# Kernel tuning notes

Hardware: AMD Instinct MI355X
Metric: run time of the kernel (lower is better)

The kernel has to match this reference:

```python
import jax, jax.numpy as jnp
from jax import lax
import numpy as np

VOCAB, EMB, HID, NLAYERS, NCLS = 32000, 512, 1024, 2, 32000
B, T = 64, 256


def setup_inputs() -> dict:
    key = jax.random.key(0)
    ks = jax.random.split(key, 12)
    s_in = 1.0 / np.sqrt(HID)
    inp = {
        "tokens": jax.random.randint(ks[0], (B, T), 0, VOCAB),
        "emb": jax.random.normal(ks[1], (VOCAB, EMB), jnp.float32),
        "W_ih0": jax.random.uniform(ks[2], (4 * HID, EMB), jnp.float32, -s_in, s_in),
        "W_hh0": jax.random.uniform(ks[3], (4 * HID, HID), jnp.float32, -s_in, s_in),
        "b_ih0": jax.random.uniform(ks[4], (4 * HID,), jnp.float32, -s_in, s_in),
        "b_hh0": jax.random.uniform(ks[5], (4 * HID,), jnp.float32, -s_in, s_in),
        "W_ih1": jax.random.uniform(ks[6], (4 * HID, HID), jnp.float32, -s_in, s_in),
        "W_hh1": jax.random.uniform(ks[7], (4 * HID, HID), jnp.float32, -s_in, s_in),
        "b_ih1": jax.random.uniform(ks[8], (4 * HID,), jnp.float32, -s_in, s_in),
        "b_hh1": jax.random.uniform(ks[9], (4 * HID,), jnp.float32, -s_in, s_in),
        "fc_w": jax.random.uniform(ks[10], (NCLS, HID), jnp.float32, -s_in, s_in),
        "fc_b": jax.random.uniform(ks[11], (NCLS,), jnp.float32, -s_in, s_in),
    }
    return inp


def _lstm_layer(x, W_ih, W_hh, b_ih, b_hh):
    # x: [B, T, in]; PyTorch gate order i, f, g, o
    Bb = x.shape[0]
    H = W_hh.shape[1]
    # precompute input-to-hidden contribution for all timesteps (one big GEMM)
    xg = jnp.einsum('bti,gi->btg', x, W_ih) + b_ih + b_hh  # [B, T, 4H]

    def step(carry, xg_t):
        h, c = carry
        g = xg_t + h @ W_hh.T  # [B, 4H]
        i, f, gg, o = jnp.split(g, 4, axis=-1)
        i = jax.nn.sigmoid(i)
        f = jax.nn.sigmoid(f)
        gg = jnp.tanh(gg)
        o = jax.nn.sigmoid(o)
        c = f * c + i * gg
        h = o * jnp.tanh(c)
        return (h, c), h

    h0 = jnp.zeros((Bb, H), x.dtype)
    (_, _), hs = lax.scan(step, (h0, h0), jnp.swapaxes(xg, 0, 1))  # hs: [T, B, H]
    return jnp.swapaxes(hs, 0, 1)


def reference(tokens, emb, W_ih0, W_hh0, b_ih0, b_hh0, W_ih1, W_hh1, b_ih1, b_hh1, fc_w, fc_b):
    x = emb[tokens]  # [B, T, EMB]
    x = _lstm_layer(x, W_ih0, W_hh0, b_ih0, b_hh0)
    x = _lstm_layer(x, W_ih1, W_hh1, b_ih1, b_hh1)
    return x[:, -1, :] @ fc_w.T + fc_b  # [B, NCLS]
```

## Files before the change

### kernel.cpp

```cpp
#include <hip/hip_runtime.h>
#include <hip/hip_bf16.h>

#define B_ 64
#define T_ 256
#define EMB_ 512
#define HID_ 1024
#define G4_ 4096
#define NCLS_ 32000
#define BH (B_ * HID_)

typedef _Float16 f16;
typedef _Float16 f16x8 __attribute__((ext_vector_type(8)));
typedef _Float16 f16x4 __attribute__((ext_vector_type(4)));
typedef float f32x4 __attribute__((ext_vector_type(4)));
typedef unsigned long long u64;

__device__ __forceinline__ float sigm(float x) { return 1.f / (1.f + __expf(-x)); }

__device__ __forceinline__ void stg_u64(u64* p, u64 v) {
  __hip_atomic_store(p, v, __ATOMIC_RELAXED, __HIP_MEMORY_SCOPE_AGENT);
}
__device__ __forceinline__ unsigned ldg_u32(const unsigned* p) {
  return __hip_atomic_load(p, __ATOMIC_RELAXED, __HIP_MEMORY_SCOPE_AGENT);
}
__device__ __forceinline__ void fadd_u32(unsigned* p) {
  __hip_atomic_fetch_add(p, 1u, __ATOMIC_RELAXED, __HIP_MEMORY_SCOPE_AGENT);
}


__global__ __launch_bounds__(256) void cvt_kernel(const float* __restrict__ src,
                                                  f16* __restrict__ dst, int n4) {
  int i = blockIdx.x * 256 + threadIdx.x;
  if (i < n4) {
    float4 v = ((const float4*)src)[i];
    f16x4 o = {(f16)v.x, (f16)v.y, (f16)v.z, (f16)v.w};
    *(f16x4*)(dst + (size_t)i * 4) = o;
  }
}

__global__ __launch_bounds__(256) void bsum_kernel(const float* __restrict__ a0,
                                                   const float* __restrict__ b0,
                                                   float* __restrict__ o0,
                                                   const float* __restrict__ a1,
                                                   const float* __restrict__ b1,
                                                   float* __restrict__ o1) {
  int i = blockIdx.x * 256 + threadIdx.x;
  if (i < G4_) {
    o0[i] = a0[i] + b0[i];
    o1[i] = a1[i] + b1[i];
  }
}

__global__ __launch_bounds__(128) void gather_kernel(const int* __restrict__ tokens,
                                                     const float* __restrict__ emb,
                                                     f16* __restrict__ x0) {
  int blk = blockIdx.x;
  int t = blk >> 6, b = blk & 63;
  int tok = tokens[b * T_ + t];
  float4 v = ((const float4*)(emb + (size_t)tok * EMB_))[threadIdx.x];
  f16x4 o = {(f16)v.x, (f16)v.y, (f16)v.z, (f16)v.w};
  *(f16x4*)(x0 + (size_t)blk * EMB_ + threadIdx.x * 4) = o;
}

#define KPH(AP, ASTR, WCOL0, ACOL0, N)                                          \
  _Pragma("unroll") for (int f = 0; f < (N); ++f) {                             \
    const f16* ap0 = (AP) + (size_t)r0 * (ASTR) + ((ACOL0) + f) * 32 + lk * 8;  \
    const f16* ap1 = (AP) + (size_t)r1 * (ASTR) + ((ACOL0) + f) * 32 + lk * 8;  \
    f16x8 a0 = *(const f16x8*)ap0;                                              \
    f16x8 a1 = *(const f16x8*)ap1;                                              \
    f16x8 b0 = *(const f16x8*)(wr0 + ((WCOL0) + f) * 32);                       \
    f16x8 b1 = *(const f16x8*)(wr1 + ((WCOL0) + f) * 32);                       \
    acc00 = __builtin_amdgcn_mfma_f32_16x16x32_f16(a0, b0, acc00, 0, 0, 0);     \
    acc01 = __builtin_amdgcn_mfma_f32_16x16x32_f16(a0, b1, acc01, 0, 0, 0);     \
    acc10 = __builtin_amdgcn_mfma_f32_16x16x32_f16(a1, b0, acc10, 0, 0, 0);     \
    acc11 = __builtin_amdgcn_mfma_f32_16x16x32_f16(a1, b1, acc11, 0, 0, 0);     \
  }

#define KPHB(AP, WCOL0, AG0, N)                                                 \
  _Pragma("unroll") for (int f = 0; f < (N); ++f) {                             \
    const f16* ap0 = (AP) + (((AG0) + f) * 4 + lk) * 512 + r0 * 8;              \
    const f16* ap1 = (AP) + (((AG0) + f) * 4 + lk) * 512 + r1 * 8;              \
    f16x8 a0 = *(const f16x8*)ap0;                                              \
    f16x8 a1 = *(const f16x8*)ap1;                                              \
    f16x8 b0 = *(const f16x8*)(wr0 + ((WCOL0) + f) * 32);                       \
    f16x8 b1 = *(const f16x8*)(wr1 + ((WCOL0) + f) * 32);                       \
    acc00 = __builtin_amdgcn_mfma_f32_16x16x32_f16(a0, b0, acc00, 0, 0, 0);     \
    acc01 = __builtin_amdgcn_mfma_f32_16x16x32_f16(a0, b1, acc01, 0, 0, 0);     \
    acc10 = __builtin_amdgcn_mfma_f32_16x16x32_f16(a1, b0, acc10, 0, 0, 0);     \
    acc11 = __builtin_amdgcn_mfma_f32_16x16x32_f16(a1, b1, acc11, 0, 0, 0);     \
  }

#define WAITS(ADDR, TGT)                                                    \
  {                                                                         \
    const unsigned tg_ = (TGT);                                             \
    unsigned v_ = ldg_u32(ADDR);                                            \
    int it_ = 0;                                                            \
    while (v_ < tg_) {                                                      \
      if (++it_ > 4000000) break;    \
      __builtin_amdgcn_s_sleep(2);                                          \
      v_ = ldg_u32(ADDR);                                                   \
    }                                                                       \
  }

__global__ __launch_bounds__(512, 2) void persist_kernel(
    const f16* __restrict__ x0, const f16* __restrict__ w0i,
    const f16* __restrict__ w0h, const f16* __restrict__ w1i,
    const f16* __restrict__ w1h, const float* __restrict__ b0s,
    const float* __restrict__ b1s, f16* __restrict__ h0r,
    f16* __restrict__ h1r, unsigned* flags) {
  __shared__ f16 Ws[32 * 2056];
  __shared__ float red[6 * 64 * 17];
  __shared__ float cst[512];

  const int layer = blockIdx.x >> 7;
  const int slice = blockIdx.x & 127;
  const int sector = slice >> 4;
  const int tid = threadIdx.x;
  const int lane = tid & 63, wave = tid >> 6;
  const int mi = wave >> 2, kq = wave & 3;
  const int lr = lane & 15, lk = lane >> 4;
  const int j0 = slice * 8;

  const f16* whh = layer ? w1h : w0h;
  const f16* wih = layer ? w1i : w0i;
  const float* bs = layer ? b1s : b0s;
  f16* hown = layer ? h1r : h0r;
  const int KI = layer ? HID_ : EMB_;
  const int nch = (HID_ + KI) >> 3;
  const int wstr = HID_ + KI + 8;

  unsigned* ctr_own = flags + (layer ? 256 : 0);
  unsigned* ctr_l0 = flags;

  for (int r = wave * 4; r < wave * 4 + 4; ++r) {
    int grow = (r >> 3) * HID_ + j0 + (r & 7);
    for (int c = lane; c < nch; c += 64) {
      int kk = c * 8;
      const f16* src = (kk < HID_) ? (whh + (size_t)grow * HID_ + kk)
                                   : (wih + (size_t)grow * KI + (kk - HID_));
      *(uint4*)(Ws + r * wstr + kk) = *(const uint4*)src;
    }
  }
  float brg[4][4];
  {
    int u4 = (tid & 1) * 4;
#pragma unroll
    for (int g = 0; g < 4; ++g)
#pragma unroll
      for (int e = 0; e < 4; ++e) brg[g][e] = bs[g * HID_ + j0 + u4 + e];
  }
  for (int i = tid; i < 512; i += 512) cst[i] = 0.f;
  __syncthreads();

  const int r0 = mi * 32 + lr, r1 = r0 + 16;
  const f16* wr0 = Ws + lr * wstr + lk * 8;
  const f16* wr1 = wr0 + 16 * wstr;

  for (int s = 0; s < T_; ++s) {
    f32x4 acc00 = {}, acc01 = {}, acc10 = {}, acc11 = {};

    if (layer == 0) {
      const f16* xb = x0 + (size_t)s * (B_ * EMB_);
      KPH(xb, EMB_, 32 + kq * 4, kq * 4, 4)
      const f16* hb = h0r + (size_t)s * BH;
#pragma unroll
      for (int sq = 0; sq < 2; ++sq) {
        int sec = kq * 2 + sq;
        WAITS(ctr_own + sec * 32, 16u * (unsigned)s)
        KPHB(hb, sec * 4, sec * 4, 4)
      }
    } else {
      const f16* xb = h0r + (size_t)(s + 1) * BH;
#pragma unroll
      for (int sq = 0; sq < 2; ++sq) {
        int sec = kq * 2 + sq;
        WAITS(ctr_l0 + sec * 32, 16u * (unsigned)(s + 1))
        KPHB(xb, 32 + sec * 4, sec * 4, 4)
      }
      const f16* hb = h1r + (size_t)s * BH;
#pragma unroll
      for (int sq = 0; sq < 2; ++sq) {
        int sec = kq * 2 + sq;
        WAITS(ctr_own + sec * 32, 16u * (unsigned)s)
        KPHB(hb, sec * 4, sec * 4, 4)
      }
    }

    if (kq) {
      float* rp = red + ((mi * 3 + kq - 1) * 64 + lane) * 17;
      *(f32x4*)(rp) = acc00;      *(f32x4*)(rp + 4) = acc01;
      *(f32x4*)(rp + 8) = acc10;  *(f32x4*)(rp + 12) = acc11;
    }
    __syncthreads();
    if (!kq) {
#pragma unroll
      for (int q = 0; q < 3; ++q) {
        const float* rp = red + ((mi * 3 + q) * 64 + lane) * 17;
        acc00 += *(const f32x4*)(rp);      acc01 += *(const f32x4*)(rp + 4);
        acc10 += *(const f32x4*)(rp + 8);  acc11 += *(const f32x4*)(rp + 12);
      }
    }
    __syncthreads();
    if (!kq) {
      float* pre = red;
      int col = mi * 32 + lk * 4;
      *(f32x4*)(pre + (0 + lr) * 68 + col) = acc00;
      *(f32x4*)(pre + (16 + lr) * 68 + col) = acc01;
      *(f32x4*)(pre + (0 + lr) * 68 + col + 16) = acc10;
      *(f32x4*)(pre + (16 + lr) * 68 + col + 16) = acc11;
    }
    __syncthreads();

    if (tid < 128) {
      const float* pre = red;
      f16* hout = hown + (size_t)(s + 1) * BH;
      int b = tid >> 1, u4 = (tid & 1) * 4;
      f16x4 hv;
#pragma unroll
      for (int e = 0; e < 4; ++e) {
        int r = u4 + e;
        float pi = pre[(0 * 8 + r) * 68 + b] + brg[0][e];
        float pf = pre[(1 * 8 + r) * 68 + b] + brg[1][e];
        float pg = pre[(2 * 8 + r) * 68 + b] + brg[2][e];
        float po = pre[(3 * 8 + r) * 68 + b] + brg[3][e];
        float ig = sigm(pi), fg = sigm(pf), gg = tanhf(pg), og = sigm(po);
        float cn = fg * cst[b * 8 + r] + ig * gg;
        cst[b * 8 + r] = cn;
        hv[e] = (f16)(og * tanhf(cn));
      }
      stg_u64((u64*)(hout + slice * 512 + b * 8 + u4),
              __builtin_bit_cast(u64, hv));
    }

    asm volatile("s_waitcnt vmcnt(0)" ::: "memory");
    __syncthreads();
    if (tid == 0) fadd_u32(&ctr_own[sector * 32]);
  }
}

__global__ __launch_bounds__(256) void fc_kernel(const f16* __restrict__ A,
                                                 const float* __restrict__ fcw,
                                                 const float* __restrict__ fcb,
                                                 float* __restrict__ out) {
  const int n0 = blockIdx.x * 64;
  __shared__ char smem[18432];
  f16* As = (f16*)smem;
  f16* Bs = (f16*)(smem + 9216);
  const int tid = threadIdx.x;
  const int lane = tid & 63, wave = tid >> 6;
  const int wm = wave & 1, wn = wave >> 1;
  const int lr = lane & 15, lk = lane >> 4;
  f32x4 acc[2][2] = {};

  for (int kt = 0; kt < HID_ / 64; ++kt) {
    const int k0 = kt * 64;
    __syncthreads();
#pragma unroll
    for (int i = 0; i < 2; ++i) {
      int id = tid + 256 * i;
      int r = id >> 3, c8 = id & 7;
      uint4 av = *(const uint4*)(A + (size_t)((k0 >> 3) + c8) * 512 + r * 8);
      *(uint4*)(As + r * 72 + c8 * 8) = av;
    }
#pragma unroll
    for (int i = 0; i < 4; ++i) {
      int id = tid + 256 * i;
      int r = id >> 4, c4 = id & 15;
      float4 v = *(const float4*)(fcw + (size_t)(n0 + r) * HID_ + k0 + c4 * 4);
      f16x4 o = {(f16)v.x, (f16)v.y, (f16)v.z, (f16)v.w};
      *(f16x4*)(Bs + r * 72 + c4 * 4) = o;
    }
    __syncthreads();
#pragma unroll
    for (int ks = 0; ks < 2; ++ks) {
      f16x8 a0 = *(const f16x8*)(As + (wm * 32 + lr) * 72 + ks * 32 + lk * 8);
      f16x8 a1 = *(const f16x8*)(As + (wm * 32 + 16 + lr) * 72 + ks * 32 + lk * 8);
      f16x8 b0 = *(const f16x8*)(Bs + (wn * 32 + lr) * 72 + ks * 32 + lk * 8);
      f16x8 b1 = *(const f16x8*)(Bs + (wn * 32 + 16 + lr) * 72 + ks * 32 + lk * 8);
      acc[0][0] = __builtin_amdgcn_mfma_f32_16x16x32_f16(a0, b0, acc[0][0], 0, 0, 0);
      acc[0][1] = __builtin_amdgcn_mfma_f32_16x16x32_f16(a0, b1, acc[0][1], 0, 0, 0);
      acc[1][0] = __builtin_amdgcn_mfma_f32_16x16x32_f16(a1, b0, acc[1][0], 0, 0, 0);
      acc[1][1] = __builtin_amdgcn_mfma_f32_16x16x32_f16(a1, b1, acc[1][1], 0, 0, 0);
    }
  }

#pragma unroll
  for (int mf = 0; mf < 2; ++mf)
#pragma unroll
    for (int nf = 0; nf < 2; ++nf) {
      int n = n0 + wn * 32 + nf * 16 + lr;
      float bias = fcb[n];
      int bbase = wm * 32 + mf * 16 + lk * 4;
#pragma unroll
      for (int rg = 0; rg < 4; ++rg)
        out[(size_t)(bbase + rg) * NCLS_ + n] = acc[mf][nf][rg] + bias;
    }
}


extern "C" void kernel_launch(void* const* d_in, const int* in_sizes, int n_in,
                              void* d_out, int out_size, void* d_ws,
                              size_t ws_size, hipStream_t stream) {
  const int* tokens = (const int*)d_in[0];
  const float* emb = (const float*)d_in[1];
  const float* W_ih0 = (const float*)d_in[2];
  const float* W_hh0 = (const float*)d_in[3];
  const float* b_ih0 = (const float*)d_in[4];
  const float* b_hh0 = (const float*)d_in[5];
  const float* W_ih1 = (const float*)d_in[6];
  const float* W_hh1 = (const float*)d_in[7];
  const float* b_ih1 = (const float*)d_in[8];
  const float* b_hh1 = (const float*)d_in[9];
  const float* fc_w = (const float*)d_in[10];
  const float* fc_b = (const float*)d_in[11];
  float* out = (float*)d_out;

  char* ws = (char*)d_ws;
  size_t off = 0;
  auto carve = [&](size_t bytes) -> char* {
    char* p = ws + off;
    off += (bytes + 255) & ~(size_t)255;
    return p;
  };
  f16* w0i = (f16*)carve((size_t)G4_ * EMB_ * 2);
  f16* w0h = (f16*)carve((size_t)G4_ * HID_ * 2);
  f16* w1i = (f16*)carve((size_t)G4_ * HID_ * 2);
  f16* w1h = (f16*)carve((size_t)G4_ * HID_ * 2);
  f16* x0 = (f16*)carve((size_t)T_ * B_ * EMB_ * 2);
  float* b0s = (float*)carve(G4_ * 4);
  float* b1s = (float*)carve(G4_ * 4);
  f16* h0r = (f16*)carve(257ull * BH * 2);
  f16* h1r = (f16*)carve(257ull * BH * 2);
  unsigned* flags = (unsigned*)carve(1024 * 4);

  hipMemsetAsync(flags, 0, 1024 * 4, stream);
  hipMemsetAsync(h0r, 0, (size_t)BH * 2, stream);
  hipMemsetAsync(h1r, 0, (size_t)BH * 2, stream);

  cvt_kernel<<<(G4_ * EMB_ / 4 + 255) / 256, 256, 0, stream>>>(W_ih0, w0i, G4_ * EMB_ / 4);
  cvt_kernel<<<(G4_ * HID_ / 4 + 255) / 256, 256, 0, stream>>>(W_hh0, w0h, G4_ * HID_ / 4);
  cvt_kernel<<<(G4_ * HID_ / 4 + 255) / 256, 256, 0, stream>>>(W_ih1, w1i, G4_ * HID_ / 4);
  cvt_kernel<<<(G4_ * HID_ / 4 + 255) / 256, 256, 0, stream>>>(W_hh1, w1h, G4_ * HID_ / 4);
  bsum_kernel<<<(G4_ + 255) / 256, 256, 0, stream>>>(b_ih0, b_hh0, b0s, b_ih1, b_hh1, b1s);
  gather_kernel<<<T_ * B_, 128, 0, stream>>>(tokens, emb, x0);

  persist_kernel<<<256, 512, 0, stream>>>(x0, w0i, w0h, w1i, w1h, b0s, b1s,
                                          h0r, h1r, flags);

  fc_kernel<<<NCLS_ / 64, 256, 0, stream>>>(h1r + 256ull * BH, fc_w, fc_b, out);
}
```

Before: 1.831 ms.

## Add fast-path readiness check and per-wave counter increments in LSTM recurrence

Before loading the hidden-state sectors, each wave polls all relevant sector counters at once. If every one is already ready, it runs a single merged 8-chunk MFMA phase instead of two wait-then-compute halves. The end-of-step block barrier is removed; each writing wave now issues its own counter increment after its stores drain, so counter targets double (32 per step instead of 16). This aims to cut synchronization latency on the serial timestep chain, at the cost of more atomics and reliance on per-wave memory ordering.

```diff
diff --git a/kernel.cpp b/kernel.cpp
--- a/kernel.cpp
+++ b/kernel.cpp
@@ -163,26 +163,52 @@
       const f16* xb = x0 + (size_t)s * (B_ * EMB_);
       KPH(xb, EMB_, 32 + kq * 4, kq * 4, 4)
       const f16* hb = h0r + (size_t)s * BH;
-#pragma unroll
-      for (int sq = 0; sq < 2; ++sq) {
-        int sec = kq * 2 + sq;
-        WAITS(ctr_own + sec * 32, 16u * (unsigned)s)
-        KPHB(hb, sec * 4, sec * 4, 4)
+      const unsigned tgo = 32u * (unsigned)s;
+      bool fast;
+      {
+        unsigned v = tgo;
+        if (lane < 2) v = ldg_u32(ctr_own + (kq * 2 + lane) * 32);
+        fast = __all((int)(v >= tgo));
+      }
+      if (fast) {
+        KPHB(hb, kq * 8, kq * 8, 8)
+      } else {
+#pragma unroll
+        for (int sq = 0; sq < 2; ++sq) {
+          int sec = kq * 2 + sq;
+          WAITS(ctr_own + sec * 32, tgo)
+          KPHB(hb, sec * 4, sec * 4, 4)
+        }
       }
     } else {
       const f16* xb = h0r + (size_t)(s + 1) * BH;
-#pragma unroll
-      for (int sq = 0; sq < 2; ++sq) {
-        int sec = kq * 2 + sq;
-        WAITS(ctr_l0 + sec * 32, 16u * (unsigned)(s + 1))
-        KPHB(xb, 32 + sec * 4, sec * 4, 4)
-      }
       const f16* hb = h1r + (size_t)s * BH;
-#pragma unroll
-      for (int sq = 0; sq < 2; ++sq) {
-        int sec = kq * 2 + sq;
-        WAITS(ctr_own + sec * 32, 16u * (unsigned)s)
-        KPHB(hb, sec * 4, sec * 4, 4)
+      const unsigned tgl0 = 32u * (unsigned)(s + 1);
+      const unsigned tgo = 32u * (unsigned)s;
+      bool fast;
+      {
+        unsigned mytg = (lane < 2) ? tgl0 : tgo;
+        unsigned v = mytg;
+        if (lane < 2) v = ldg_u32(ctr_l0 + (kq * 2 + lane) * 32);
+        else if (lane < 4) v = ldg_u32(ctr_own + (kq * 2 + (lane - 2)) * 32);
+        fast = __all((int)(v >= mytg));
+      }
+      if (fast) {
+        KPHB(xb, 32 + kq * 8, kq * 8, 8)
+        KPHB(hb, kq * 8, kq * 8, 8)
+      } else {
+#pragma unroll
+        for (int sq = 0; sq < 2; ++sq) {
+          int sec = kq * 2 + sq;
+          WAITS(ctr_l0 + sec * 32, tgl0)
+          KPHB(xb, 32 + sec * 4, sec * 4, 4)
+        }
+#pragma unroll
+        for (int sq = 0; sq < 2; ++sq) {
+          int sec = kq * 2 + sq;
+          WAITS(ctr_own + sec * 32, tgo)
+          KPHB(hb, sec * 4, sec * 4, 4)
+        }
       }
     }
 
@@ -230,11 +256,9 @@
       }
       stg_u64((u64*)(hout + slice * 512 + b * 8 + u4),
               __builtin_bit_cast(u64, hv));
-    }
-
-    asm volatile("s_waitcnt vmcnt(0)" ::: "memory");
-    __syncthreads();
-    if (tid == 0) fadd_u32(&ctr_own[sector * 32]);
+      asm volatile("s_waitcnt vmcnt(0)" ::: "memory");
+      if (lane == 0) fadd_u32(&ctr_own[sector * 32]);
+    }
   }
 }
 
```

New measurement: 2.484 ms. +35.7%, slower.
